# Optimization experiments

Measured on AMD Instinct MI355X. Metric: run time of the kernel, lower is better.

## Reference

```python
import jax, jax.numpy as jnp
import numpy as np

N = 16384          # number of input points
K = 16             # kNN neighbors for EdgeConv
SCALES = (4096, 1024, 256)
DIM = 256
EC_HID = 64        # EdgeConv output dim
MLP_HID = 128


def _sqdist(a, b):
    # squared euclidean distance matrix: (Na, Nb)
    return (jnp.sum(a * a, axis=1, keepdims=True)
            - 2.0 * (a @ b.T)
            + jnp.sum(b * b, axis=1)[None, :])


def _fps(points, n):
    # farthest point sampling, deterministic start at index 0
    d = jnp.sum((points - points[0]) ** 2, axis=1)  # (N,)

    def step(d, _):
        nxt = jnp.argmax(d)
        d = jnp.minimum(d, jnp.sum((points - points[nxt]) ** 2, axis=1))
        return d, nxt

    _, rest = jax.lax.scan(step, d, None, length=n - 1)
    return jnp.concatenate([jnp.zeros((1,), dtype=rest.dtype), rest])


def setup_inputs() -> dict:
    key = jax.random.key(0)
    ks = jax.random.split(key, 10)

    def lin(k, fi, fo):
        return (jax.random.normal(k, (fi, fo), jnp.float32) / np.sqrt(fi)).astype(jnp.float32)

    nsc = len(SCALES)
    return {
        "points": jax.random.normal(ks[0], (N, 3), jnp.float32),
        # EdgeConv MLP: Linear(6,64) -> ReLU -> Linear(64,64)
        "ew1": lin(ks[1], 6, EC_HID), "eb1": jnp.zeros((EC_HID,), jnp.float32),
        "ew2": lin(ks[2], EC_HID, EC_HID), "eb2": jnp.zeros((EC_HID,), jnp.float32),
        # per-scale MLPs: Linear(64,128) -> ReLU -> Linear(128,256), stacked over scales
        "mw1": jnp.stack([lin(jax.random.fold_in(ks[3], i), EC_HID, MLP_HID) for i in range(nsc)]),
        "mb1": jnp.zeros((nsc, MLP_HID), jnp.float32),
        "mw2": jnp.stack([lin(jax.random.fold_in(ks[4], i), MLP_HID, DIM) for i in range(nsc)]),
        "mb2": jnp.zeros((nsc, DIM), jnp.float32),
    }


def _edge_conv(points, ew1, eb1, ew2, eb2):
    # kNN graph (loop=False): exclude self via +inf diagonal; indices not differentiated
    d = jax.lax.stop_gradient(_sqdist(points, points))
    d = d.at[jnp.arange(N), jnp.arange(N)].set(jnp.inf)
    _, idx = jax.lax.top_k(-d, K)                      # (N, K) neighbor indices
    x_i = points[:, None, :]                           # (N, 1, 3) centers
    x_j = points[idx]                                  # (N, K, 3) neighbors
    ef = jnp.concatenate([jnp.broadcast_to(x_i, (N, K, 3)), x_j - x_i], axis=-1)  # (N,K,6)
    h = jax.nn.relu(ef @ ew1 + eb1) @ ew2 + eb2        # (N, K, 64)
    # scatter_max over centers == max over the K neighbor axis (every center has K edges)
    return jnp.max(h, axis=1)                          # (N, 64)


def reference(points, ew1, eb1, ew2, eb2, mw1, mb1, mw2, mb2):
    feats = _edge_conv(points, ew1, eb1, ew2, eb2)     # (N, 64)
    outs = []
    prev_pts = None
    for i, scale in enumerate(SCALES):
        if i == 0:
            fi = _fps(points, scale)
            sp = points[fi]
            sf = feats[fi]
        else:
            fi = _fps(prev_pts, scale)
            sp = prev_pts[fi]
            nn = jnp.argmin(_sqdist(sp, points), axis=1)  # nearest source point per query
            sf = feats[nn]
        lf = jax.nn.relu(sf @ mw1[i] + mb1[i]) @ mw2[i] + mb2[i]  # (scale, DIM)
        outs.append(sp)
        outs.append(lf)
        prev_pts = sp
    return tuple(outs)
```

## Files before the change

### kernel.cpp

```cpp
#include <hip/hip_runtime.h>
#include <cfloat>
#include <cstdint>

#define N_PTS 16384
#define KNN_K 16
#define KNN_TILE 512
#define CERT_EPS 3e-6f

struct FpsSmem {
    unsigned long long slots[2][16];
    int cw2[2][2];
    float4 pub;
    int cand_idx[64];
    int cand_cnt;
    int more_flag;
    double red_d[16];
};

template <int CTRL>
__device__ __forceinline__ unsigned dpp_mov_u32(unsigned v) {
    return (unsigned)__builtin_amdgcn_update_dpp((int)v, (int)v, CTRL, 0xF, 0xF, false);
}

__device__ __forceinline__ void cross_slot_reduce(unsigned long long k, float& M1, int& G1) {
    unsigned hi = (unsigned)(k >> 32), lo = (unsigned)k;
#define RSTEP(CTRL)                                          \
    {                                                        \
        const unsigned ohi = dpp_mov_u32<CTRL>(hi);          \
        const unsigned olo = dpp_mov_u32<CTRL>(lo);          \
        const bool b = (ohi > hi) || (ohi == hi && olo > lo);\
        hi = b ? ohi : hi;                                   \
        lo = b ? olo : lo;                                   \
    }
    RSTEP(0x121)
    RSTEP(0x122)
    RSTEP(0x124)
    RSTEP(0x128)
#undef RSTEP
    M1 = __uint_as_float(hi);
    G1 = (int)(~lo);
}

__device__ __forceinline__ void fps_run(FpsSmem& sm, const float* __restrict__ pts,
                                        int n_out, int* __restrict__ fi) {
    constexpr int T = 1024;
    constexpr int P = 16;
    constexpr int NW = T / 64;
    const int tid = threadIdx.x;
    const int wave = tid >> 6, lane = tid & 63;

    if (tid < 32) sm.slots[tid >> 4][tid & 15] = 0ull;
    if (tid < 4) sm.cw2[tid >> 1][tid & 1] = 0;

    float xr[P], yr[P], zr[P], c[P];
    const float sx0 = pts[0], sy0 = pts[1], sz0 = pts[2];
    if (tid == 0) fi[0] = 0;

    float m1 = -1.0f;
    int g1 = 0x7fffffff;
#pragma unroll
    for (int q = 0; q < P; ++q) {
        const int g = tid + q * T;
        const float x = pts[g * 3 + 0];
        const float y = pts[g * 3 + 1];
        const float z = pts[g * 3 + 2];
        xr[q] = x;
        yr[q] = y;
        zr[q] = z;
        const float dx = x - sx0, dy = y - sy0, dz = z - sz0;
        const float t = fmaf(dx, dx, fmaf(dy, dy, dz * dz));
        const float nc = fminf(FLT_MAX, t);
        c[q] = nc;
        const bool gt = nc > m1;
        m1 = fmaxf(m1, nc);
        g1 = gt ? g : g1;
    }
    __syncthreads();
    {
        const unsigned long long key =
            ((unsigned long long)__float_as_uint(m1) << 32) |
            (unsigned long long)(~(unsigned)g1);
        atomicMax(&sm.slots[1][tid & 15], key);
    }

    for (int s = 1; s < n_out; ++s) {
        __syncthreads();
        const int par = s & 1;

        const unsigned long long k0 = sm.slots[par][lane & 15];
        float M1;
        int G1;
        cross_slot_reduce(k0, M1, G1);
        const float thr = M1 - M1 * CERT_EPS;

        if (g1 == G1) {
            const int qw = (G1 - tid) >> 10;
            float xw = 0.0f, yw = 0.0f, zw = 0.0f, m2w = -1.0f;
#pragma unroll
            for (int q = 0; q < P; ++q) {
                if (q == qw) { xw = xr[q]; yw = yr[q]; zw = zr[q]; }
                else m2w = fmaxf(m2w, c[q]);
            }
            sm.pub = make_float4(xw, yw, zw, 0.0f);
            sm.cw2[par][1] = (m2w >= thr) ? 1 : 0;
        }

        if (tid < 16) sm.slots[par ^ 1][tid] = 0ull;
        if (tid == 0) { sm.cw2[par ^ 1][0] = 0; sm.cw2[par ^ 1][1] = 0; }

        const unsigned long long bal = __ballot(m1 >= thr);
        if (lane == 0) atomicAdd(&sm.cw2[par][0], (int)__popcll(bal));

        __syncthreads();
        const int2 tw = *reinterpret_cast<const int2*>(&sm.cw2[par][0]);
        const int total = tw.x, wfl = tw.y;
        const float4 wc = sm.pub;
        float nx = wc.x, ny = wc.y, nz = wc.z;
        int wg = G1;

        if (total > 1 || wfl) {
            unsigned miss = 0;
#pragma unroll
            for (int q = 0; q < P; ++q)
                if (c[q] >= thr) miss |= (1u << q);
            double BD = -1.0;
            int BG = 0x7fffffff;
            for (;;) {
                if (tid == 0) { sm.cand_cnt = 0; sm.more_flag = 0; }
                __syncthreads();
#pragma unroll
                for (int q = 0; q < P; ++q) {
                    if (miss & (1u << q)) {
                        int slot = atomicAdd(&sm.cand_cnt, 1);
                        if (slot < 64) {
                            sm.cand_idx[slot] = tid + q * T;
                            miss &= ~(1u << q);
                        } else {
                            sm.more_flag = 1;
                        }
                    }
                }
                __syncthreads();
                int ncand = sm.cand_cnt;
                if (ncand > 64) ncand = 64;
                for (int ci = 0; ci < ncand; ++ci) {
                    const int g = sm.cand_idx[ci];
                    const double qx = (double)pts[g * 3 + 0];
                    const double qy = (double)pts[g * 3 + 1];
                    const double qz = (double)pts[g * 3 + 2];
                    double dmin = DBL_MAX;
                    for (int i = tid; i < s; i += T) {
                        const int h = fi[i];
                        double ddx = qx - (double)pts[h * 3 + 0];
                        double ddy = qy - (double)pts[h * 3 + 1];
                        double ddz = qz - (double)pts[h * 3 + 2];
                        double dd = ddx * ddx + ddy * ddy + ddz * ddz;
                        dmin = (dd < dmin) ? dd : dmin;
                    }
                    for (int off = 32; off; off >>= 1) {
                        double od = __shfl_xor(dmin, off);
                        dmin = (od < dmin) ? od : dmin;
                    }
                    if (lane == 0) sm.red_d[wave] = dmin;
                    __syncthreads();
                    double dall = sm.red_d[0];
#pragma unroll
                    for (int w = 1; w < NW; ++w) dall = (sm.red_d[w] < dall) ? sm.red_d[w] : dall;
                    if (dall > BD || (dall == BD && g < BG)) { BD = dall; BG = g; }
                    __syncthreads();
                }
                int mf = sm.more_flag;
                __syncthreads();
                if (!mf) break;
            }
            wg = BG;
            nx = pts[wg * 3 + 0];
            ny = pts[wg * 3 + 1];
            nz = pts[wg * 3 + 2];
        }

        if (tid == 0) fi[s] = wg;
        if (s == n_out - 1) break;

        float nm1 = -1.0f;
        int ng1 = 0x7fffffff;
#pragma unroll
        for (int q = 0; q < P; ++q) {
            const float dx = xr[q] - nx, dy = yr[q] - ny, dz = zr[q] - nz;
            const float t = fmaf(dx, dx, fmaf(dy, dy, dz * dz));
            const float nc = fminf(c[q], t);
            c[q] = nc;
            const bool gt = nc > nm1;
            nm1 = fmaxf(nm1, nc);
            ng1 = gt ? (tid + q * T) : ng1;
        }
        m1 = nm1; g1 = ng1;
        const unsigned long long key =
            ((unsigned long long)__float_as_uint(m1) << 32) |
            (unsigned long long)(~(unsigned)g1);
        atomicMax(&sm.slots[par ^ 1][tid & 15], key);
    }
}

struct KnnSmem {
    float sx[KNN_TILE], sy[KNN_TILE], sz[KNN_TILE];
    float w1[6 * 64], b1v[64], w2[64 * 64], b2v[64];
};

__device__ __forceinline__ void knn_edge_body(
    KnnSmem& sm, const float* __restrict__ pts,
    const float* __restrict__ ew1, const float* __restrict__ eb1,
    const float* __restrict__ ew2, const float* __restrict__ eb2,
    float* __restrict__ feats, int qb) {
    for (int t = threadIdx.x; t < 6 * 64; t += 1024) sm.w1[t] = ew1[t];
    for (int t = threadIdx.x; t < 64; t += 1024) { sm.b1v[t] = eb1[t]; sm.b2v[t] = eb2[t]; }
    for (int t = threadIdx.x; t < 64 * 64; t += 1024) sm.w2[t] = ew2[t];

    const int wave = threadIdx.x >> 6;
    const int lane = threadIdx.x & 63;
    const int qi = qb * 16 + wave;
    const double qxd = (double)pts[qi * 3 + 0];
    const double qyd = (double)pts[qi * 3 + 1];
    const double qzd = (double)pts[qi * 3 + 2];

    double ld[16];
    int li[16];
#pragma unroll
    for (int s = 0; s < 16; ++s) { ld[s] = DBL_MAX; li[s] = 0x7fffffff; }
    double md = DBL_MAX; int mj = 0x7fffffff; int mslot = 0;

    for (int t0 = 0; t0 < N_PTS; t0 += KNN_TILE) {
        __syncthreads();
        for (int t = threadIdx.x; t < KNN_TILE; t += 1024) {
            sm.sx[t] = pts[(t0 + t) * 3 + 0];
            sm.sy[t] = pts[(t0 + t) * 3 + 1];
            sm.sz[t] = pts[(t0 + t) * 3 + 2];
        }
        __syncthreads();
#pragma unroll
        for (int m = 0; m < KNN_TILE / 64; ++m) {
            const int cc = lane + m * 64;
            const int j = t0 + cc;
            if (j == qi) continue;
            double dx = qxd - (double)sm.sx[cc];
            double dy = qyd - (double)sm.sy[cc];
            double dz = qzd - (double)sm.sz[cc];
            double dd = dx * dx + dy * dy + dz * dz;
            if (dd < md || (dd == md && j < mj)) {
#pragma unroll
                for (int s = 0; s < 16; ++s)
                    if (s == mslot) { ld[s] = dd; li[s] = j; }
                md = -1.0; mj = -1; mslot = 0;
#pragma unroll
                for (int s = 0; s < 16; ++s) {
                    bool g = (ld[s] > md) || (ld[s] == md && li[s] > mj);
                    if (g) { md = ld[s]; mj = li[s]; mslot = s; }
                }
            }
        }
    }

    const float xi = pts[qi * 3], yi = pts[qi * 3 + 1], zi = pts[qi * 3 + 2];
    float acc = -FLT_MAX;
    for (int r = 0; r < KNN_K; ++r) {
        double cd = DBL_MAX; int cj = 0x7fffffff; int cs = 0;
#pragma unroll
        for (int s = 0; s < 16; ++s) {
            bool l = (ld[s] < cd) || (ld[s] == cd && li[s] < cj);
            if (l) { cd = ld[s]; cj = li[s]; cs = s; }
        }
        double wd = cd; int wj = cj;
        for (int off = 32; off; off >>= 1) {
            double od = __shfl_xor(wd, off);
            int oj = __shfl_xor(wj, off);
            if (od < wd || (od == wd && oj < wj)) { wd = od; wj = oj; }
        }
        if (cd == wd && cj == wj) {
#pragma unroll
            for (int s = 0; s < 16; ++s)
                if (s == cs) { ld[s] = DBL_MAX; li[s] = 0x7fffffff; }
        }
        const float xj = pts[wj * 3], yj = pts[wj * 3 + 1], zj = pts[wj * 3 + 2];
        const float f3 = xj - xi, f4 = yj - yi, f5 = zj - zi;
        float h1 = sm.b1v[lane];
        h1 = fmaf(xi, sm.w1[0 * 64 + lane], h1);
        h1 = fmaf(yi, sm.w1[1 * 64 + lane], h1);
        h1 = fmaf(zi, sm.w1[2 * 64 + lane], h1);
        h1 = fmaf(f3, sm.w1[3 * 64 + lane], h1);
        h1 = fmaf(f4, sm.w1[4 * 64 + lane], h1);
        h1 = fmaf(f5, sm.w1[5 * 64 + lane], h1);
        h1 = fmaxf(h1, 0.0f);
        float h2 = sm.b2v[lane];
        for (int d = 0; d < 64; ++d)
            h2 = fmaf(__shfl(h1, d), sm.w2[d * 64 + lane], h2);
        acc = fmaxf(acc, h2);
    }
    feats[qi * 64 + lane] = acc;
}

__global__ __launch_bounds__(1024)
void mega_kernel(const float* __restrict__ pts,
                 const float* __restrict__ ew1, const float* __restrict__ eb1,
                 const float* __restrict__ ew2, const float* __restrict__ eb2,
                 float* __restrict__ feats,
                 int* __restrict__ fi0,
                 float* __restrict__ sp0, float* __restrict__ sp1,
                 float* __restrict__ sp2) {
    constexpr size_t SMEM_BYTES =
        sizeof(FpsSmem) > sizeof(KnnSmem) ? sizeof(FpsSmem) : sizeof(KnnSmem);
    __shared__ __align__(16) char raw[SMEM_BYTES];
    if (blockIdx.x == 0) {
        FpsSmem& sm = *reinterpret_cast<FpsSmem*>(raw);
        fps_run(sm, pts, 4096, fi0);
        __syncthreads();
        const int tid = threadIdx.x;
        for (int t = tid; t < 4096; t += 1024) {
            const int g = fi0[t];
            const float x = pts[g * 3 + 0];
            const float y = pts[g * 3 + 1];
            const float z = pts[g * 3 + 2];
            sp0[t * 3 + 0] = x;
            sp0[t * 3 + 1] = y;
            sp0[t * 3 + 2] = z;
            if (t < 1024) {
                sp1[t * 3 + 0] = x;
                sp1[t * 3 + 1] = y;
                sp1[t * 3 + 2] = z;
            }
            if (t < 256) {
                sp2[t * 3 + 0] = x;
                sp2[t * 3 + 1] = y;
                sp2[t * 3 + 2] = z;
            }
        }
    } else {
        knn_edge_body(*reinterpret_cast<KnnSmem*>(raw), pts, ew1, eb1, ew2, eb2,
                      feats, blockIdx.x - 1);
    }
}

__device__ __forceinline__ void mlp_body(
    const float* __restrict__ feats, const int* __restrict__ orig,
    const float* __restrict__ mw1, const float* __restrict__ mb1,
    const float* __restrict__ mw2, const float* __restrict__ mb2,
    float* __restrict__ outp, int pb) {
    __shared__ float sfl[64], h1l[128];
    const int t = threadIdx.x;
    for (int pl = 0; pl < 16; ++pl) {
        const int p = pb * 16 + pl;
        const int g = orig[p];
        if (t < 64) sfl[t] = feats[g * 64 + t];
        __syncthreads();
        if (t < 128) {
            float h = mb1[t];
            for (int dd = 0; dd < 64; ++dd)
                h = fmaf(sfl[dd], mw1[dd * 128 + t], h);
            h1l[t] = fmaxf(h, 0.0f);
        }
        __syncthreads();
        float o = mb2[t];
        for (int dd = 0; dd < 128; ++dd)
            o = fmaf(h1l[dd], mw2[dd * 256 + t], o);
        outp[p * 256 + t] = o;
        __syncthreads();
    }
}

__global__ __launch_bounds__(256) void tail_kernel(
    const float* __restrict__ feats,
    const int* __restrict__ fi0,
    const float* __restrict__ mw1, const float* __restrict__ mb1,
    const float* __restrict__ mw2, const float* __restrict__ mb2,
    float* __restrict__ out) {
    const int b = blockIdx.x;
    float* lf0 = out + 12288;
    float* lf1 = out + 1063936;
    float* lf2 = out + 1326848;
    if (b < 256) {
        mlp_body(feats, fi0, mw1 + 0 * 8192, mb1 + 0 * 128,
                 mw2 + 0 * 32768, mb2 + 0 * 256, lf0, b);
    } else if (b < 320) {
        mlp_body(feats, fi0, mw1 + 1 * 8192, mb1 + 1 * 128,
                 mw2 + 1 * 32768, mb2 + 1 * 256, lf1, b - 256);
    } else {
        mlp_body(feats, fi0, mw1 + 2 * 8192, mb1 + 2 * 128,
                 mw2 + 2 * 32768, mb2 + 2 * 256, lf2, b - 320);
    }
}

extern "C" void kernel_launch(void* const* d_in, const int* in_sizes, int n_in,
                              void* d_out, int out_size, void* d_ws, size_t ws_size,
                              hipStream_t stream) {
    const float* pts = (const float*)d_in[0];
    const float* ew1 = (const float*)d_in[1];
    const float* eb1 = (const float*)d_in[2];
    const float* ew2 = (const float*)d_in[3];
    const float* eb2 = (const float*)d_in[4];
    const float* mw1 = (const float*)d_in[5];
    const float* mb1 = (const float*)d_in[6];
    const float* mw2 = (const float*)d_in[7];
    const float* mb2 = (const float*)d_in[8];
    float* out = (float*)d_out;
    char* ws = (char*)d_ws;

    float* feats = (float*)(ws + 0);
    int* fi0 = (int*)(ws + 4194304);

    float* sp0 = out + 0;
    float* sp1 = out + 1060864;
    float* sp2 = out + 1326080;

    mega_kernel<<<1 + N_PTS / 16, 1024, 0, stream>>>(pts, ew1, eb1, ew2, eb2, feats,
                                                     fi0, sp0, sp1, sp2);
    tail_kernel<<<336, 256, 0, stream>>>(feats, fi0, mw1, mb1, mw2, mb2, out);
}
```

Measured before the change: 6.845 ms.

## Shrink FPS block to 512 threads with DPP wave reduction and LDS-staged MLP

The mega kernel now runs 512-thread blocks, so the serial FPS block uses 8 waves with 32 points per thread. The per-iteration shared-memory atomicMax into 16 slots is replaced by a full-wave DPP reduction that writes one key per wave, which also removes the slot zeroing. The kNN/EdgeConv blocks handle 8 queries each, and the second MLP layer reads h1 from LDS as float4 instead of using 64 shuffles. The intent is to cut barrier and atomic latency in the serial FPS critical path, at the cost of doubled per-thread register arrays (risking spills) and twice as many kNN blocks.

```diff
diff --git a/kernel.cpp b/kernel.cpp
--- a/kernel.cpp
+++ b/kernel.cpp
@@ -8,18 +8,38 @@
 #define CERT_EPS 3e-6f
 
 struct FpsSmem {
-    unsigned long long slots[2][16];
+    unsigned long long slots[2][8];
     int cw2[2][2];
     float4 pub;
     int cand_idx[64];
     int cand_cnt;
     int more_flag;
-    double red_d[16];
+    double red_d[8];
 };
 
 template <int CTRL>
 __device__ __forceinline__ unsigned dpp_mov_u32(unsigned v) {
     return (unsigned)__builtin_amdgcn_update_dpp((int)v, (int)v, CTRL, 0xF, 0xF, false);
+}
+
+__device__ __forceinline__ unsigned long long wave_reduce_key(unsigned long long k) {
+    unsigned hi = (unsigned)(k >> 32), lo = (unsigned)k;
+#define WSTEP(CTRL)                                          \
+    {                                                        \
+        const unsigned ohi = dpp_mov_u32<CTRL>(hi);          \
+        const unsigned olo = dpp_mov_u32<CTRL>(lo);          \
+        const bool b = (ohi > hi) || (ohi == hi && olo > lo);\
+        hi = b ? ohi : hi;                                   \
+        lo = b ? olo : lo;                                   \
+    }
+    WSTEP(0x121)
+    WSTEP(0x122)
+    WSTEP(0x124)
+    WSTEP(0x128)
+    WSTEP(0x142)
+    WSTEP(0x143)
+#undef WSTEP
+    return ((unsigned long long)hi << 32) | (unsigned long long)lo;
 }
 
 __device__ __forceinline__ void cross_slot_reduce(unsigned long long k, float& M1, int& G1) {
@@ -35,7 +55,6 @@
     RSTEP(0x121)
     RSTEP(0x122)
     RSTEP(0x124)
-    RSTEP(0x128)
 #undef RSTEP
     M1 = __uint_as_float(hi);
     G1 = (int)(~lo);
@@ -43,13 +62,12 @@
 
 __device__ __forceinline__ void fps_run(FpsSmem& sm, const float* __restrict__ pts,
                                         int n_out, int* __restrict__ fi) {
-    constexpr int T = 1024;
-    constexpr int P = 16;
+    constexpr int T = 512;
+    constexpr int P = 32;
     constexpr int NW = T / 64;
     const int tid = threadIdx.x;
     const int wave = tid >> 6, lane = tid & 63;
 
-    if (tid < 32) sm.slots[tid >> 4][tid & 15] = 0ull;
     if (tid < 4) sm.cw2[tid >> 1][tid & 1] = 0;
 
     float xr[P], yr[P], zr[P], c[P];
@@ -75,26 +93,26 @@
         m1 = fmaxf(m1, nc);
         g1 = gt ? g : g1;
     }
-    __syncthreads();
     {
         const unsigned long long key =
             ((unsigned long long)__float_as_uint(m1) << 32) |
             (unsigned long long)(~(unsigned)g1);
-        atomicMax(&sm.slots[1][tid & 15], key);
+        const unsigned long long wk = wave_reduce_key(key);
+        if (lane == 63) sm.slots[1][wave] = wk;
     }
 
     for (int s = 1; s < n_out; ++s) {
         __syncthreads();
         const int par = s & 1;
 
-        const unsigned long long k0 = sm.slots[par][lane & 15];
+        const unsigned long long k0 = sm.slots[par][lane & 7];
         float M1;
         int G1;
         cross_slot_reduce(k0, M1, G1);
         const float thr = M1 - M1 * CERT_EPS;
 
         if (g1 == G1) {
-            const int qw = (G1 - tid) >> 10;
+            const int qw = (G1 - tid) >> 9;
             float xw = 0.0f, yw = 0.0f, zw = 0.0f, m2w = -1.0f;
 #pragma unroll
             for (int q = 0; q < P; ++q) {
@@ -105,7 +123,6 @@
             sm.cw2[par][1] = (m2w >= thr) ? 1 : 0;
         }
 
-        if (tid < 16) sm.slots[par ^ 1][tid] = 0ull;
         if (tid == 0) { sm.cw2[par ^ 1][0] = 0; sm.cw2[par ^ 1][1] = 0; }
 
         const unsigned long long bal = __ballot(m1 >= thr);
@@ -198,13 +215,15 @@
         const unsigned long long key =
             ((unsigned long long)__float_as_uint(m1) << 32) |
             (unsigned long long)(~(unsigned)g1);
-        atomicMax(&sm.slots[par ^ 1][tid & 15], key);
+        const unsigned long long wk = wave_reduce_key(key);
+        if (lane == 63) sm.slots[par ^ 1][wave] = wk;
     }
 }
 
 struct KnnSmem {
     float sx[KNN_TILE], sy[KNN_TILE], sz[KNN_TILE];
     float w1[6 * 64], b1v[64], w2[64 * 64], b2v[64];
+    __align__(16) float h1buf[8][64];
 };
 
 __device__ __forceinline__ void knn_edge_body(
@@ -212,13 +231,13 @@
     const float* __restrict__ ew1, const float* __restrict__ eb1,
     const float* __restrict__ ew2, const float* __restrict__ eb2,
     float* __restrict__ feats, int qb) {
-    for (int t = threadIdx.x; t < 6 * 64; t += 1024) sm.w1[t] = ew1[t];
-    for (int t = threadIdx.x; t < 64; t += 1024) { sm.b1v[t] = eb1[t]; sm.b2v[t] = eb2[t]; }
-    for (int t = threadIdx.x; t < 64 * 64; t += 1024) sm.w2[t] = ew2[t];
+    for (int t = threadIdx.x; t < 6 * 64; t += 512) sm.w1[t] = ew1[t];
+    for (int t = threadIdx.x; t < 64; t += 512) { sm.b1v[t] = eb1[t]; sm.b2v[t] = eb2[t]; }
+    for (int t = threadIdx.x; t < 64 * 64; t += 512) sm.w2[t] = ew2[t];
 
     const int wave = threadIdx.x >> 6;
     const int lane = threadIdx.x & 63;
-    const int qi = qb * 16 + wave;
+    const int qi = qb * 8 + wave;
     const double qxd = (double)pts[qi * 3 + 0];
     const double qyd = (double)pts[qi * 3 + 1];
     const double qzd = (double)pts[qi * 3 + 2];
@@ -231,7 +250,7 @@
 
     for (int t0 = 0; t0 < N_PTS; t0 += KNN_TILE) {
         __syncthreads();
-        for (int t = threadIdx.x; t < KNN_TILE; t += 1024) {
+        for (int t = threadIdx.x; t < KNN_TILE; t += 512) {
             sm.sx[t] = pts[(t0 + t) * 3 + 0];
             sm.sy[t] = pts[(t0 + t) * 3 + 1];
             sm.sz[t] = pts[(t0 + t) * 3 + 2];
@@ -290,15 +309,23 @@
         h1 = fmaf(f4, sm.w1[4 * 64 + lane], h1);
         h1 = fmaf(f5, sm.w1[5 * 64 + lane], h1);
         h1 = fmaxf(h1, 0.0f);
+        sm.h1buf[wave][lane] = h1;
         float h2 = sm.b2v[lane];
-        for (int d = 0; d < 64; ++d)
-            h2 = fmaf(__shfl(h1, d), sm.w2[d * 64 + lane], h2);
+        const float4* h4 = reinterpret_cast<const float4*>(&sm.h1buf[wave][0]);
+#pragma unroll
+        for (int dd = 0; dd < 16; ++dd) {
+            const float4 hv = h4[dd];
+            h2 = fmaf(hv.x, sm.w2[(dd * 4 + 0) * 64 + lane], h2);
+            h2 = fmaf(hv.y, sm.w2[(dd * 4 + 1) * 64 + lane], h2);
+            h2 = fmaf(hv.z, sm.w2[(dd * 4 + 2) * 64 + lane], h2);
+            h2 = fmaf(hv.w, sm.w2[(dd * 4 + 3) * 64 + lane], h2);
+        }
         acc = fmaxf(acc, h2);
     }
     feats[qi * 64 + lane] = acc;
 }
 
-__global__ __launch_bounds__(1024)
+__global__ __launch_bounds__(512, 2)
 void mega_kernel(const float* __restrict__ pts,
                  const float* __restrict__ ew1, const float* __restrict__ eb1,
                  const float* __restrict__ ew2, const float* __restrict__ eb2,
@@ -314,7 +341,7 @@
         fps_run(sm, pts, 4096, fi0);
         __syncthreads();
         const int tid = threadIdx.x;
-        for (int t = tid; t < 4096; t += 1024) {
+        for (int t = tid; t < 4096; t += 512) {
             const int g = fi0[t];
             const float x = pts[g * 3 + 0];
             const float y = pts[g * 3 + 1];
@@ -410,7 +437,7 @@
     float* sp1 = out + 1060864;
     float* sp2 = out + 1326080;
 
-    mega_kernel<<<1 + N_PTS / 16, 1024, 0, stream>>>(pts, ew1, eb1, ew2, eb2, feats,
-                                                     fi0, sp0, sp1, sp2);
+    mega_kernel<<<1 + N_PTS / 8, 512, 0, stream>>>(pts, ew1, eb1, ew2, eb2, feats,
+                                                   fi0, sp0, sp1, sp2);
     tail_kernel<<<336, 256, 0, stream>>>(feats, fi0, mw1, mb1, mw2, mb2, out);
 }
```

New measurement: 8.156 ms. 1.19x slower.

## Spatially sort FPS points per thread and skip distance updates for far threads

Applied to the files above, without the earlier changes.

Before FPS starts, the points are bucketed into a Morton-ordered grid through an in-block histogram, prefix scan and scatter, so each thread holds 16 spatially nearby points. Each thread keeps a bounding sphere around its points and skips the per-step distance update when the new sample is provably too far to lower any of its distances, which cuts ALU work in the serial FPS loop. Tie-breaking now compares original indices explicitly to keep argmax semantics. Separately, the EdgeConv second layer reads h1 from LDS as float4 instead of doing 64 shuffles. The cost is a larger shared-memory footprint for FPS (a 16K-entry index array) and extra setup work.

```diff
diff --git a/kernel.cpp b/kernel.cpp
--- a/kernel.cpp
+++ b/kernel.cpp
@@ -8,6 +8,10 @@
 #define CERT_EPS 3e-6f
 
 struct FpsSmem {
+    int sorted[N_PTS];
+    int hist[2048];
+    int wsum[16];
+    float bred[16][6];
     unsigned long long slots[2][16];
     int cw2[2][2];
     float4 pub;
@@ -49,39 +53,120 @@
     const int tid = threadIdx.x;
     const int wave = tid >> 6, lane = tid & 63;
 
+    float mnx = FLT_MAX, mny = FLT_MAX, mnz = FLT_MAX;
+    float mxx = -FLT_MAX, mxy = -FLT_MAX, mxz = -FLT_MAX;
+#pragma unroll
+    for (int q = 0; q < P; ++q) {
+        const int g = tid + q * T;
+        const float x = pts[g * 3], y = pts[g * 3 + 1], z = pts[g * 3 + 2];
+        mnx = fminf(mnx, x); mny = fminf(mny, y); mnz = fminf(mnz, z);
+        mxx = fmaxf(mxx, x); mxy = fmaxf(mxy, y); mxz = fmaxf(mxz, z);
+    }
+    for (int off = 32; off; off >>= 1) {
+        mnx = fminf(mnx, __shfl_xor(mnx, off));
+        mny = fminf(mny, __shfl_xor(mny, off));
+        mnz = fminf(mnz, __shfl_xor(mnz, off));
+        mxx = fmaxf(mxx, __shfl_xor(mxx, off));
+        mxy = fmaxf(mxy, __shfl_xor(mxy, off));
+        mxz = fmaxf(mxz, __shfl_xor(mxz, off));
+    }
+    if (lane == 0) {
+        sm.bred[wave][0] = mnx; sm.bred[wave][1] = mny; sm.bred[wave][2] = mnz;
+        sm.bred[wave][3] = mxx; sm.bred[wave][4] = mxy; sm.bred[wave][5] = mxz;
+    }
+    sm.hist[tid] = 0;
+    sm.hist[tid + 1024] = 0;
     if (tid < 32) sm.slots[tid >> 4][tid & 15] = 0ull;
     if (tid < 4) sm.cw2[tid >> 1][tid & 1] = 0;
+    __syncthreads();
+#pragma unroll
+    for (int w = 0; w < NW; ++w) {
+        mnx = fminf(mnx, sm.bred[w][0]); mny = fminf(mny, sm.bred[w][1]);
+        mnz = fminf(mnz, sm.bred[w][2]);
+        mxx = fmaxf(mxx, sm.bred[w][3]); mxy = fmaxf(mxy, sm.bred[w][4]);
+        mxz = fmaxf(mxz, sm.bred[w][5]);
+    }
+    const float sclx = 15.9999f / fmaxf(mxx - mnx, 1e-30f);
+    const float scly = 15.9999f / fmaxf(mxy - mny, 1e-30f);
+    const float sclz = 7.9999f / fmaxf(mxz - mnz, 1e-30f);
+    auto mkey = [&](float x, float y, float z) -> int {
+        int kx = (int)((x - mnx) * sclx); kx = kx < 0 ? 0 : (kx > 15 ? 15 : kx);
+        int ky = (int)((y - mny) * scly); ky = ky < 0 ? 0 : (ky > 15 ? 15 : ky);
+        int kz = (int)((z - mnz) * sclz); kz = kz < 0 ? 0 : (kz > 7 ? 7 : kz);
+        return ((kx & 8) << 7) | ((ky & 8) << 6) | ((kz & 4) << 6) |
+               ((kx & 4) << 5) | ((ky & 4) << 4) | ((kz & 2) << 4) |
+               ((kx & 2) << 3) | ((ky & 2) << 2) | ((kz & 1) << 2) |
+               ((kx & 1) << 1) | (ky & 1);
+    };
+#pragma unroll
+    for (int q = 0; q < P; ++q) {
+        const int g = tid + q * T;
+        atomicAdd(&sm.hist[mkey(pts[g * 3], pts[g * 3 + 1], pts[g * 3 + 2])], 1);
+    }
+    __syncthreads();
+    {
+        const int a = sm.hist[2 * tid], b = sm.hist[2 * tid + 1];
+        const int tsum = a + b;
+        int v = tsum;
+        for (int off = 1; off < 64; off <<= 1) {
+            const int o = __shfl_up(v, off);
+            if (lane >= off) v += o;
+        }
+        if (lane == 63) sm.wsum[wave] = v;
+        __syncthreads();
+        int wbase = 0;
+#pragma unroll
+        for (int w = 0; w < NW; ++w) wbase += (w < wave) ? sm.wsum[w] : 0;
+        const int ex = wbase + v - tsum;
+        sm.hist[2 * tid] = ex;
+        sm.hist[2 * tid + 1] = ex + a;
+    }
+    __syncthreads();
+#pragma unroll
+    for (int q = 0; q < P; ++q) {
+        const int g = tid + q * T;
+        const int k = mkey(pts[g * 3], pts[g * 3 + 1], pts[g * 3 + 2]);
+        const int pos = atomicAdd(&sm.hist[k], 1);
+        sm.sorted[pos] = g;
+    }
+    __syncthreads();
 
     float xr[P], yr[P], zr[P], c[P];
     const float sx0 = pts[0], sy0 = pts[1], sz0 = pts[2];
     if (tid == 0) fi[0] = 0;
-
+    float Cx = 0.0f, Cy = 0.0f, Cz = 0.0f, r2max = 0.0f;
     float m1 = -1.0f;
-    int g1 = 0x7fffffff;
+    int g1 = 0x7fffffff, q1 = 0;
 #pragma unroll
     for (int q = 0; q < P; ++q) {
-        const int g = tid + q * T;
-        const float x = pts[g * 3 + 0];
-        const float y = pts[g * 3 + 1];
-        const float z = pts[g * 3 + 2];
-        xr[q] = x;
-        yr[q] = y;
-        zr[q] = z;
+        const int gg = sm.sorted[tid * P + q];
+        const float x = pts[gg * 3], y = pts[gg * 3 + 1], z = pts[gg * 3 + 2];
+        xr[q] = x; yr[q] = y; zr[q] = z;
+        if (q == 0) { Cx = x; Cy = y; Cz = z; }
+        const float rdx = x - Cx, rdy = y - Cy, rdz = z - Cz;
+        r2max = fmaxf(r2max, fmaf(rdx, rdx, fmaf(rdy, rdy, rdz * rdz)));
         const float dx = x - sx0, dy = y - sy0, dz = z - sz0;
         const float t = fmaf(dx, dx, fmaf(dy, dy, dz * dz));
         const float nc = fminf(FLT_MAX, t);
         c[q] = nc;
-        const bool gt = nc > m1;
-        m1 = fmaxf(m1, nc);
-        g1 = gt ? g : g1;
-    }
-    __syncthreads();
+        const bool gt = (nc > m1) || (nc == m1 && gg < g1);
+        m1 = gt ? nc : m1;
+        g1 = gt ? gg : g1;
+        q1 = gt ? q : q1;
+    }
+    const float R_safe = sqrtf(r2max) * 1.000004f;
     {
-        const unsigned long long key =
-            ((unsigned long long)__float_as_uint(m1) << 32) |
-            (unsigned long long)(~(unsigned)g1);
-        atomicMax(&sm.slots[1][tid & 15], key);
-    }
+        const float srt = R_safe + sqrtf(fmaxf(m1, 0.0f)) * 1.000004f;
+    }
+    float SR2;
+    {
+        const float srt = R_safe + sqrtf(fmaxf(m1, 0.0f)) * 1.000004f;
+        SR2 = srt * srt * 1.000008f;
+    }
+    unsigned long long ckey =
+        ((unsigned long long)__float_as_uint(m1) << 32) |
+        (unsigned long long)(~(unsigned)g1);
+    atomicMax(&sm.slots[1][tid & 15], ckey);
 
     for (int s = 1; s < n_out; ++s) {
         __syncthreads();
@@ -94,11 +179,10 @@
         const float thr = M1 - M1 * CERT_EPS;
 
         if (g1 == G1) {
-            const int qw = (G1 - tid) >> 10;
             float xw = 0.0f, yw = 0.0f, zw = 0.0f, m2w = -1.0f;
 #pragma unroll
             for (int q = 0; q < P; ++q) {
-                if (q == qw) { xw = xr[q]; yw = yr[q]; zw = zr[q]; }
+                if (q == q1) { xw = xr[q]; yw = yr[q]; zw = zr[q]; }
                 else m2w = fmaxf(m2w, c[q]);
             }
             sm.pub = make_float4(xw, yw, zw, 0.0f);
@@ -133,7 +217,7 @@
                     if (miss & (1u << q)) {
                         int slot = atomicAdd(&sm.cand_cnt, 1);
                         if (slot < 64) {
-                            sm.cand_idx[slot] = tid + q * T;
+                            sm.cand_idx[slot] = sm.sorted[tid * P + q];
                             miss &= ~(1u << q);
                         } else {
                             sm.more_flag = 1;
@@ -182,29 +266,37 @@
         if (tid == 0) fi[s] = wg;
         if (s == n_out - 1) break;
 
-        float nm1 = -1.0f;
-        int ng1 = 0x7fffffff;
-#pragma unroll
-        for (int q = 0; q < P; ++q) {
-            const float dx = xr[q] - nx, dy = yr[q] - ny, dz = zr[q] - nz;
-            const float t = fmaf(dx, dx, fmaf(dy, dy, dz * dz));
-            const float nc = fminf(c[q], t);
-            c[q] = nc;
-            const bool gt = nc > nm1;
-            nm1 = fmaxf(nm1, nc);
-            ng1 = gt ? (tid + q * T) : ng1;
-        }
-        m1 = nm1; g1 = ng1;
-        const unsigned long long key =
-            ((unsigned long long)__float_as_uint(m1) << 32) |
-            (unsigned long long)(~(unsigned)g1);
-        atomicMax(&sm.slots[par ^ 1][tid & 15], key);
+        const float pdx = Cx - nx, pdy = Cy - ny, pdz = Cz - nz;
+        const float d2cn = fmaf(pdx, pdx, fmaf(pdy, pdy, pdz * pdz));
+        if (!__all(d2cn >= SR2)) {
+            float nm1 = -1.0f;
+            int ng1 = 0x7fffffff, nq1 = 0;
+#pragma unroll
+            for (int q = 0; q < P; ++q) {
+                const float dx = xr[q] - nx, dy = yr[q] - ny, dz = zr[q] - nz;
+                const float t = fmaf(dx, dx, fmaf(dy, dy, dz * dz));
+                const float nc = fminf(c[q], t);
+                c[q] = nc;
+                const int og = sm.sorted[tid * P + q];
+                const bool gt = (nc > nm1) || (nc == nm1 && og < ng1);
+                nm1 = gt ? nc : nm1;
+                ng1 = gt ? og : ng1;
+                nq1 = gt ? q : nq1;
+            }
+            m1 = nm1; g1 = ng1; q1 = nq1;
+            ckey = ((unsigned long long)__float_as_uint(m1) << 32) |
+                   (unsigned long long)(~(unsigned)g1);
+            const float srt = R_safe + sqrtf(m1) * 1.000004f;
+            SR2 = srt * srt * 1.000008f;
+        }
+        atomicMax(&sm.slots[par ^ 1][tid & 15], ckey);
     }
 }
 
 struct KnnSmem {
     float sx[KNN_TILE], sy[KNN_TILE], sz[KNN_TILE];
     float w1[6 * 64], b1v[64], w2[64 * 64], b2v[64];
+    __align__(16) float h1buf[16][64];
 };
 
 __device__ __forceinline__ void knn_edge_body(
@@ -290,9 +382,17 @@
         h1 = fmaf(f4, sm.w1[4 * 64 + lane], h1);
         h1 = fmaf(f5, sm.w1[5 * 64 + lane], h1);
         h1 = fmaxf(h1, 0.0f);
+        sm.h1buf[wave][lane] = h1;
         float h2 = sm.b2v[lane];
-        for (int d = 0; d < 64; ++d)
-            h2 = fmaf(__shfl(h1, d), sm.w2[d * 64 + lane], h2);
+        const float4* h4 = reinterpret_cast<const float4*>(&sm.h1buf[wave][0]);
+#pragma unroll
+        for (int dd = 0; dd < 16; ++dd) {
+            const float4 hv = h4[dd];
+            h2 = fmaf(hv.x, sm.w2[(dd * 4 + 0) * 64 + lane], h2);
+            h2 = fmaf(hv.y, sm.w2[(dd * 4 + 1) * 64 + lane], h2);
+            h2 = fmaf(hv.z, sm.w2[(dd * 4 + 2) * 64 + lane], h2);
+            h2 = fmaf(hv.w, sm.w2[(dd * 4 + 3) * 64 + lane], h2);
+        }
         acc = fmaxf(acc, h2);
     }
     feats[qi * 64 + lane] = acc;
```

Result: slower. 14.89 ms (+117.6%).
